# Performance work log

Hardware: AMD Instinct MI355X
Metric: run time of the kernel (lower is better)

Reference implementation:

```python
import jax, jax.numpy as jnp
import numpy as np

B, S, E2, E = 2, 512, 512, 256  # batch, seq, 2*encode_size, encode_size


def setup_inputs() -> dict:
    key = jax.random.key(0)
    k1, k2, k3, k4 = jax.random.split(key, 4)
    query = jax.random.normal(k1, (B, S, E2), dtype=jnp.float32)
    value = jax.random.normal(k2, (B, S, E2), dtype=jnp.float32)
    # nn.Linear weights (no bias); stored as [in, out] for x @ W convention
    Wd = jax.random.normal(k3, (E2, E), dtype=jnp.float32) * (1.0 / np.sqrt(E2))
    vd = jax.random.normal(k4, (E,), dtype=jnp.float32) * (1.0 / np.sqrt(E))
    return {"query": query, "value": value, "Wd": Wd, "vd": vd}


def reference(query, value, Wd, vd):
    # q = query.unsqueeze(1) -> [B,1,S,2E]; k = query.unsqueeze(2) -> [B,S,1,2E]
    # NOTE: original module ignores its `key` arg; both factors come from query.
    qk = query[:, None, :, :] * query[:, :, None, :]        # [B,S,S,2E]
    h = jnp.tanh(jnp.einsum('bsth,hd->bstd', qk, Wd))        # [B,S,S,E]
    sjt = jnp.einsum('bstd,d->bst', h, vd)                   # [B,S,S]
    atten = jax.nn.softmax(sjt, axis=2)                      # softmax over dim=2
    # dropout p=0.0 -> identity
    context = jnp.einsum('bst,btd->bsd', atten, value)       # bmm
    return (context, atten)
```

## Files before the change

### kernel.cpp

```cpp
#include <hip/hip_runtime.h>

#define B_  2
#define S_  512
#define E2_ 512
#define E_  256

#define TT  64
#define KB  32
#define LDK 40

using f32x4 = __attribute__((ext_vector_type(4))) float;
using f16x8 = __attribute__((ext_vector_type(8))) _Float16;

__device__ __forceinline__ float tanh_fast(float x) {
    float e = __expf(2.0f * x);
    return 1.0f - 2.0f / (e + 1.0f);
}

#define SBAR() __builtin_amdgcn_sched_barrier(0)

__global__ void prep_all(const float* __restrict__ q, _Float16* __restrict__ qh,
                         const float* __restrict__ Wd, _Float16* __restrict__ Wp2) {
    int idx = blockIdx.x * 256 + threadIdx.x;
    float4 v = *(const float4*)(q + idx * 4);
    _Float16 h4[4] = {(_Float16)v.x, (_Float16)v.y, (_Float16)v.z, (_Float16)v.w};
    *(short4*)(qh + idx * 4) = *(short4*)h4;
    int h = idx >> 8;
    int d = idx & 255;
    int ko = h >> 5;
    int kk = h & 31;
    Wp2[ko * (E_ * KB) + d * KB + kk] = (_Float16)Wd[idx];
}

__global__ __launch_bounds__(256, 4)
void stage1(const _Float16* __restrict__ qh,
            const _Float16* __restrict__ Wp2,
            const float* __restrict__ vd,
            float* __restrict__ logits ) {
    const int x  = blockIdx.x;
    const int p  = x >> 6;
    const int sl = x & 63;
    const int b  = blockIdx.y;
    int sj = 0;
    while ((sj + 1) * (sj + 2) / 2 <= p) ++sj;
    const int ti = p - sj * (sj + 1) / 2;
    const int s  = sj * TT + sl;
    const int t0 = ti * TT;

    __shared__ _Float16 sA[2][TT * LDK];
    __shared__ _Float16 sQsh[E2_];
    __shared__ float sVd[E_];

    const int tid = threadIdx.x;
    {
        const _Float16* qsrow = qh + ((size_t)(b * S_ + s)) * E2_;
        sQsh[tid]       = qsrow[tid];
        sQsh[tid + 256] = qsrow[tid + 256];
        sVd[tid & 255]  = vd[tid & 255];
    }
    __syncthreads();

    const int wave = tid >> 6;
    const int lane = tid & 63;
    const int wd   = wave;
    const int l15  = lane & 15;
    const int l4   = lane >> 4;

    const int a_row = tid >> 2;
    const int a_g   = tid & 3;
    const int a_off = a_row * LDK + a_g * 8;
    const _Float16* qt = qh + ((size_t)(b * S_ + t0 + a_row)) * E2_ + a_g * 8;

    const _Float16* wpb = Wp2 + (wd * 64 + l15) * KB + l4 * 8;

    f16x8 ra;
    auto ALOAD  = [&](int k0) { ra = *(const f16x8*)(qt + k0); };
    auto AWRITE = [&](int k0, int hh) {
        f16x8 q = *(const f16x8*)&sQsh[k0 + a_g * 8];
        *(f16x8*)&sA[hh][a_off] = ra * q;
    };

    f32x4 acc[4][4] = {};

    ALOAD(0);
    SBAR();
    AWRITE(0, 0);
    SBAR();
    ALOAD(KB);
    SBAR();
    asm volatile("s_waitcnt lgkmcnt(0)" ::: "memory");
    __builtin_amdgcn_s_barrier();
    SBAR();

    for (int ko = 0; ko < E2_ / KB; ++ko) {
        const int h = ko & 1;
        f16x8 bf[4];
        {
            const _Float16* wk = wpb + ko * (E_ * KB);
#pragma unroll
            for (int fd = 0; fd < 4; ++fd)
                bf[fd] = *(const f16x8*)(wk + fd * 16 * KB);
        }
        SBAR();
        f16x8 af[4];
#pragma unroll
        for (int ft = 0; ft < 4; ++ft) {
            int row = ft * 16 + l15;
            af[ft] = *(const f16x8*)&sA[h][row * LDK + l4 * 8];
        }
        SBAR();
        if (ko < 15) { AWRITE((ko + 1) * KB, h ^ 1); SBAR(); }
        if (ko < 14) { ALOAD((ko + 2) * KB); SBAR(); }
        if (ko < 15) {
            asm volatile("s_waitcnt lgkmcnt(0)" ::: "memory");
            __builtin_amdgcn_s_barrier();
            SBAR();
        }
        __builtin_amdgcn_s_setprio(1);
#pragma unroll
        for (int ft = 0; ft < 4; ++ft)
#pragma unroll
            for (int fd = 0; fd < 4; ++fd)
                acc[ft][fd] = __builtin_amdgcn_mfma_f32_16x16x32_f16(af[ft], bf[fd], acc[ft][fd], 0, 0, 0);
        __builtin_amdgcn_s_setprio(0);
    }

    __syncthreads();

    float* sRed = (float*)&sA[0][0];
    {
        float vdr[4];
#pragma unroll
        for (int fd = 0; fd < 4; ++fd) vdr[fd] = sVd[wd * 64 + fd * 16 + l15];
#pragma unroll
        for (int ft = 0; ft < 4; ++ft) {
#pragma unroll
            for (int r = 0; r < 4; ++r) {
                float pp = 0.f;
#pragma unroll
                for (int fd = 0; fd < 4; ++fd)
                    pp += tanh_fast(acc[ft][fd][r]) * vdr[fd];
                pp += __shfl_xor(pp, 1);
                pp += __shfl_xor(pp, 2);
                pp += __shfl_xor(pp, 4);
                pp += __shfl_xor(pp, 8);
                if (l15 == 0) {
                    int tl = ft * 16 + l4 * 4 + r;
                    sRed[tl * 4 + wd] = pp;
                }
            }
        }
    }
    __syncthreads();
    if (tid < TT) {
        float v = sRed[tid * 4 + 0] + sRed[tid * 4 + 1] + sRed[tid * 4 + 2] + sRed[tid * 4 + 3];
        int t = t0 + tid;
        logits[((size_t)(b * S_ + s)) * S_ + t] = v;
        logits[((size_t)(b * S_ + t)) * S_ + s] = v;
    }
}

__global__ void softmax_k(float* __restrict__ atten) {
    const int row  = blockIdx.x;
    const int lane = threadIdx.x;
    float* p = atten + (size_t)row * S_;
    float4 v0 = *(float4*)(p + lane * 8);
    float4 v1 = *(float4*)(p + lane * 8 + 4);
    float vv[8] = {v0.x, v0.y, v0.z, v0.w, v1.x, v1.y, v1.z, v1.w};
    float m = vv[0];
#pragma unroll
    for (int j = 1; j < 8; ++j) m = fmaxf(m, vv[j]);
#pragma unroll
    for (int off = 1; off < 64; off <<= 1) m = fmaxf(m, __shfl_xor(m, off));
    float ssum = 0.f;
#pragma unroll
    for (int j = 0; j < 8; ++j) { vv[j] = __expf(vv[j] - m); ssum += vv[j]; }
#pragma unroll
    for (int off = 1; off < 64; off <<= 1) ssum += __shfl_xor(ssum, off);
    float inv = 1.0f / ssum;
    float4 o0 = {vv[0] * inv, vv[1] * inv, vv[2] * inv, vv[3] * inv};
    float4 o1 = {vv[4] * inv, vv[5] * inv, vv[6] * inv, vv[7] * inv};
    *(float4*)(p + lane * 8)     = o0;
    *(float4*)(p + lane * 8 + 4) = o1;
}

__global__ __launch_bounds__(256)
void context_k(const float* __restrict__ atten, const float* __restrict__ value,
               float* __restrict__ ctx) {
    __shared__ float sA[32][65];
    __shared__ float sV[64][65];
    const int b  = blockIdx.z;
    const int s0 = blockIdx.y * 32;
    const int e0 = blockIdx.x * 64;
    const int tid = threadIdx.x;
    const int ts = tid >> 4;
    const int te = tid & 15;

    float acc[2][4] = {};
    for (int k0 = 0; k0 < S_; k0 += 64) {
        {
            int r = tid >> 3;
            int c = (tid & 7) * 8;
            const float* ga = atten + ((size_t)(b * S_ + s0 + r)) * S_ + k0 + c;
            *(float4*)&sA[r][c]     = *(const float4*)ga;
            *(float4*)&sA[r][c + 4] = *(const float4*)(ga + 4);
        }
        {
            int r = tid >> 2;
            int c = (tid & 3) * 16;
            const float* gv = value + ((size_t)(b * S_ + k0 + r)) * E2_ + e0 + c;
#pragma unroll
            for (int j = 0; j < 16; j += 4)
                *(float4*)&sV[r][c + j] = *(const float4*)(gv + j);
        }
        __syncthreads();
#pragma unroll 8
        for (int kk = 0; kk < 64; ++kk) {
            float a0 = sA[ts * 2 + 0][kk];
            float a1 = sA[ts * 2 + 1][kk];
#pragma unroll
            for (int j = 0; j < 4; ++j) {
                float vvv = sV[kk][te * 4 + j];
                acc[0][j] += a0 * vvv;
                acc[1][j] += a1 * vvv;
            }
        }
        __syncthreads();
    }
#pragma unroll
    for (int i = 0; i < 2; ++i)
#pragma unroll
        for (int j = 0; j < 4; ++j)
            ctx[((size_t)(b * S_ + s0 + ts * 2 + i)) * E2_ + e0 + te * 4 + j] = acc[i][j];
}

extern "C" void kernel_launch(void* const* d_in, const int* in_sizes, int n_in,
                              void* d_out, int out_size, void* d_ws, size_t ws_size,
                              hipStream_t stream) {
    const float* query = (const float*)d_in[0];
    const float* value = (const float*)d_in[1];
    const float* Wd    = (const float*)d_in[2];
    const float* vd    = (const float*)d_in[3];

    float* out   = (float*)d_out;
    float* ctx   = out;
    float* atten = out + (size_t)B_ * S_ * E2_;

    const size_t need = (size_t)(B_ * S_ * E2_ + 16 * E_ * KB) * sizeof(_Float16);
    _Float16* qh;
    if (ws_size >= need) {
        qh = (_Float16*)d_ws;
    } else {
        qh = (_Float16*)ctx;
    }
    _Float16* wp2 = qh + (size_t)B_ * S_ * E2_;

    prep_all<<<dim3(512), dim3(256), 0, stream>>>(query, qh, Wd, wp2);
    stage1<<<dim3(2304, B_), dim3(256), 0, stream>>>(qh, wp2, vd, atten);
    softmax_k<<<dim3(B_ * S_), dim3(64), 0, stream>>>(atten);
    context_k<<<dim3(E2_ / 64, S_ / 32, B_), dim3(256), 0, stream>>>(atten, value, ctx);
}
```

Before: 141.5 us.

## Stage half of K-dimension into shared memory per barrier instead of 32-wide double buffer

Replaces the per-32-wide-slice double-buffered A staging, which needed a barrier every K step, with staging 256 columns at once into a wider LDS tile (LDK 264). Only two barrier phases remain, and the MFMA inner loop runs eight K slices per phase with no intervening synchronization. The cost is a much larger LDS footprint (about 33KB for sA), which may lower occupancy below the 4 blocks per CU targeted by launch bounds. It also drops the overlap of global loads with MFMA, since each half is loaded in bulk before compute starts.

```diff
diff --git a/kernel.cpp b/kernel.cpp
--- a/kernel.cpp
+++ b/kernel.cpp
@@ -7,7 +7,7 @@
 
 #define TT  64
 #define KB  32
-#define LDK 40
+#define LDK 264
 
 using f32x4 = __attribute__((ext_vector_type(4))) float;
 using f16x8 = __attribute__((ext_vector_type(8))) _Float16;
@@ -16,8 +16,6 @@
     float e = __expf(2.0f * x);
     return 1.0f - 2.0f / (e + 1.0f);
 }
-
-#define SBAR() __builtin_amdgcn_sched_barrier(0)
 
 __global__ void prep_all(const float* __restrict__ q, _Float16* __restrict__ qh,
                          const float* __restrict__ Wd, _Float16* __restrict__ Wp2) {
@@ -47,7 +45,7 @@
     const int s  = sj * TT + sl;
     const int t0 = ti * TT;
 
-    __shared__ _Float16 sA[2][TT * LDK];
+    __shared__ _Float16 sA[TT * LDK];
     __shared__ _Float16 sQsh[E2_];
     __shared__ float sVd[E_];
 
@@ -67,67 +65,59 @@
     const int l4   = lane >> 4;
 
     const int a_row = tid >> 2;
-    const int a_g   = tid & 3;
-    const int a_off = a_row * LDK + a_g * 8;
-    const _Float16* qt = qh + ((size_t)(b * S_ + t0 + a_row)) * E2_ + a_g * 8;
+    const int kg    = tid & 3;
+    const _Float16* qt = qh + ((size_t)(b * S_ + t0 + a_row)) * E2_;
+
+    auto STAGE_HALF = [&](int h2) {
+#pragma unroll
+        for (int g = 0; g < 8; ++g) {
+            int kl = (g * 4 + kg) * 8;
+            f16x8 t = *(const f16x8*)(qt + h2 * 256 + kl);
+            f16x8 q = *(const f16x8*)&sQsh[h2 * 256 + kl];
+            *(f16x8*)&sA[a_row * LDK + kl] = t * q;
+        }
+    };
 
     const _Float16* wpb = Wp2 + (wd * 64 + l15) * KB + l4 * 8;
 
-    f16x8 ra;
-    auto ALOAD  = [&](int k0) { ra = *(const f16x8*)(qt + k0); };
-    auto AWRITE = [&](int k0, int hh) {
-        f16x8 q = *(const f16x8*)&sQsh[k0 + a_g * 8];
-        *(f16x8*)&sA[hh][a_off] = ra * q;
-    };
-
     f32x4 acc[4][4] = {};
 
-    ALOAD(0);
-    SBAR();
-    AWRITE(0, 0);
-    SBAR();
-    ALOAD(KB);
-    SBAR();
+    STAGE_HALF(0);
     asm volatile("s_waitcnt lgkmcnt(0)" ::: "memory");
     __builtin_amdgcn_s_barrier();
-    SBAR();
-
-    for (int ko = 0; ko < E2_ / KB; ++ko) {
-        const int h = ko & 1;
-        f16x8 bf[4];
-        {
-            const _Float16* wk = wpb + ko * (E_ * KB);
+
+#pragma unroll
+    for (int h2 = 0; h2 < 2; ++h2) {
+#pragma unroll 2
+        for (int ko = 0; ko < 8; ++ko) {
+            const _Float16* wk = wpb + (h2 * 8 + ko) * (E_ * KB);
+            f16x8 bf[4], af[4];
 #pragma unroll
             for (int fd = 0; fd < 4; ++fd)
                 bf[fd] = *(const f16x8*)(wk + fd * 16 * KB);
-        }
-        SBAR();
-        f16x8 af[4];
-#pragma unroll
-        for (int ft = 0; ft < 4; ++ft) {
-            int row = ft * 16 + l15;
-            af[ft] = *(const f16x8*)&sA[h][row * LDK + l4 * 8];
-        }
-        SBAR();
-        if (ko < 15) { AWRITE((ko + 1) * KB, h ^ 1); SBAR(); }
-        if (ko < 14) { ALOAD((ko + 2) * KB); SBAR(); }
-        if (ko < 15) {
+#pragma unroll
+            for (int ft = 0; ft < 4; ++ft)
+                af[ft] = *(const f16x8*)&sA[(ft * 16 + l15) * LDK + ko * 32 + l4 * 8];
+            __builtin_amdgcn_s_setprio(1);
+#pragma unroll
+            for (int ft = 0; ft < 4; ++ft)
+#pragma unroll
+                for (int fd = 0; fd < 4; ++fd)
+                    acc[ft][fd] = __builtin_amdgcn_mfma_f32_16x16x32_f16(af[ft], bf[fd], acc[ft][fd], 0, 0, 0);
+            __builtin_amdgcn_s_setprio(0);
+        }
+        if (h2 == 0) {
             asm volatile("s_waitcnt lgkmcnt(0)" ::: "memory");
             __builtin_amdgcn_s_barrier();
-            SBAR();
-        }
-        __builtin_amdgcn_s_setprio(1);
-#pragma unroll
-        for (int ft = 0; ft < 4; ++ft)
-#pragma unroll
-            for (int fd = 0; fd < 4; ++fd)
-                acc[ft][fd] = __builtin_amdgcn_mfma_f32_16x16x32_f16(af[ft], bf[fd], acc[ft][fd], 0, 0, 0);
-        __builtin_amdgcn_s_setprio(0);
+            STAGE_HALF(1);
+            asm volatile("s_waitcnt lgkmcnt(0)" ::: "memory");
+            __builtin_amdgcn_s_barrier();
+        }
     }
 
     __syncthreads();
 
-    float* sRed = (float*)&sA[0][0];
+    float* sRed = (float*)&sA[0];
     {
         float vdr[4];
 #pragma unroll
```

Measured after the change: 147.6 us. 1.04x slower.

## Deepen stage1 LDS pipeline to four buffers and move barrier after MFMAs

Applied to the files above, without the earlier changes.

Replaces the double-buffered LDS staging of the query-product A tile with a four-slot ring, prefetching global loads three steps ahead and writing products two steps ahead. The barrier now sits after the MFMA block with a partial lgkmcnt wait, and the loop is fully unrolled with all sched_barriers removed. The aim is to hide LDS write and barrier latency behind matrix math. In exchange it doubles the A-tile LDS footprint, which may lower occupancy, and makes correctness depend on fragile waitcnt counting.

```diff
diff --git a/kernel.cpp b/kernel.cpp
--- a/kernel.cpp
+++ b/kernel.cpp
@@ -16,8 +16,6 @@
     float e = __expf(2.0f * x);
     return 1.0f - 2.0f / (e + 1.0f);
 }
-
-#define SBAR() __builtin_amdgcn_sched_barrier(0)
 
 __global__ void prep_all(const float* __restrict__ q, _Float16* __restrict__ qh,
                          const float* __restrict__ Wd, _Float16* __restrict__ Wp2) {
@@ -47,7 +45,7 @@
     const int s  = sj * TT + sl;
     const int t0 = ti * TT;
 
-    __shared__ _Float16 sA[2][TT * LDK];
+    __shared__ _Float16 sA[4][TT * LDK];
     __shared__ _Float16 sQsh[E2_];
     __shared__ float sVd[E_];
 
@@ -73,27 +71,25 @@
 
     const _Float16* wpb = Wp2 + (wd * 64 + l15) * KB + l4 * 8;
 
-    f16x8 ra;
-    auto ALOAD  = [&](int k0) { ra = *(const f16x8*)(qt + k0); };
-    auto AWRITE = [&](int k0, int hh) {
+    f16x8 ra0, ra1;
+    auto AWRITE = [&](int slot, f16x8 ra, int k0) {
         f16x8 q = *(const f16x8*)&sQsh[k0 + a_g * 8];
-        *(f16x8*)&sA[hh][a_off] = ra * q;
+        *(f16x8*)&sA[slot][a_off] = ra * q;
     };
 
     f32x4 acc[4][4] = {};
 
-    ALOAD(0);
-    SBAR();
-    AWRITE(0, 0);
-    SBAR();
-    ALOAD(KB);
-    SBAR();
+    ra0 = *(const f16x8*)(qt + 0 * KB);
+    AWRITE(0, ra0, 0 * KB);
+    ra1 = *(const f16x8*)(qt + 1 * KB);
+    AWRITE(1, ra1, 1 * KB);
+    ra0 = *(const f16x8*)(qt + 2 * KB);
     asm volatile("s_waitcnt lgkmcnt(0)" ::: "memory");
     __builtin_amdgcn_s_barrier();
-    SBAR();
-
-    for (int ko = 0; ko < E2_ / KB; ++ko) {
-        const int h = ko & 1;
+
+#pragma unroll
+    for (int ko = 0; ko < 16; ++ko) {
+        const int slot = ko & 3;
         f16x8 bf[4];
         {
             const _Float16* wk = wpb + ko * (E_ * KB);
@@ -101,20 +97,16 @@
             for (int fd = 0; fd < 4; ++fd)
                 bf[fd] = *(const f16x8*)(wk + fd * 16 * KB);
         }
-        SBAR();
         f16x8 af[4];
 #pragma unroll
         for (int ft = 0; ft < 4; ++ft) {
             int row = ft * 16 + l15;
-            af[ft] = *(const f16x8*)&sA[h][row * LDK + l4 * 8];
-        }
-        SBAR();
-        if (ko < 15) { AWRITE((ko + 1) * KB, h ^ 1); SBAR(); }
-        if (ko < 14) { ALOAD((ko + 2) * KB); SBAR(); }
-        if (ko < 15) {
-            asm volatile("s_waitcnt lgkmcnt(0)" ::: "memory");
-            __builtin_amdgcn_s_barrier();
-            SBAR();
+            af[ft] = *(const f16x8*)&sA[slot][row * LDK + l4 * 8];
+        }
+        if (ko <= 13) AWRITE((ko + 2) & 3, (ko & 1) ? ra1 : ra0, (ko + 2) * KB);
+        if (ko <= 12) {
+            if ((ko + 3) & 1) ra1 = *(const f16x8*)(qt + (ko + 3) * KB);
+            else              ra0 = *(const f16x8*)(qt + (ko + 3) * KB);
         }
         __builtin_amdgcn_s_setprio(1);
 #pragma unroll
@@ -123,6 +115,13 @@
             for (int fd = 0; fd < 4; ++fd)
                 acc[ft][fd] = __builtin_amdgcn_mfma_f32_16x16x32_f16(af[ft], bf[fd], acc[ft][fd], 0, 0, 0);
         __builtin_amdgcn_s_setprio(0);
+        if (ko <= 13) {
+            asm volatile("s_waitcnt lgkmcnt(1)" ::: "memory");
+            __builtin_amdgcn_s_barrier();
+        } else if (ko == 14) {
+            asm volatile("s_waitcnt lgkmcnt(0)" ::: "memory");
+            __builtin_amdgcn_s_barrier();
+        }
     }
 
     __syncthreads();
```

After: 143.5 us. About the same (+1.4%).
